# Kernel tuning notes

Hardware: AMD Instinct MI355X
Metric: run time of the kernel (lower is better)

Reference implementation:

```python
import jax, jax.numpy as jnp
import numpy as np

NL, D, Di, N, R, K, V, NH = 24, 768, 1536, 16, 48, 4, 50280, 12
BATCH, SEQ = 4, 256


def setup_inputs():
    key = jax.random.key(0)
    it = iter(jax.random.split(key, 48))
    g = lambda shape, s=0.02: jax.random.normal(next(it), shape, jnp.float32) * s
    inp = {
        "question_ids": jax.random.randint(next(it), (BATCH, SEQ), 0, V),
        "question_mask": jnp.ones((BATCH, SEQ), jnp.int32),
        "answer_ids": jax.random.randint(next(it), (BATCH, SEQ), 0, V),
        "answer_mask": jnp.ones((BATCH, SEQ), jnp.int32),
        "embed": g((V, D)),
        "norm_w": jnp.ones((NL, D)),
        "in_proj_w": g((NL, 2 * Di, D)),
        "conv_w": g((NL, Di, K), 0.1),
        "conv_b": jnp.zeros((NL, Di)),
        "x_proj_w": g((NL, R + 2 * N, Di)),
        "dt_proj_w": g((NL, Di, R)),
        "dt_proj_b": g((NL, Di), 0.5) - 4.0,
        "A_log": jnp.log(jnp.broadcast_to(jnp.arange(1, N + 1, dtype=jnp.float32), (NL, Di, N))) + 0.0,
        "D_p": jnp.ones((NL, Di)),
        "out_proj_w": g((NL, D, Di)),
        "norm_f": jnp.ones((D,)),
        "ln1_w": jnp.ones((D,)), "ln1_b": jnp.zeros((D,)),
        "qkv_w": g((3 * D, D)), "qkv_b": jnp.zeros((3 * D,)),
        "attn_out_w": g((D, D)), "attn_out_b": jnp.zeros((D,)),
        "ln2_w": jnp.ones((D,)), "ln2_b": jnp.zeros((D,)),
        "ff1_w": g((4 * D, D)), "ff1_b": jnp.zeros((4 * D,)),
        "ff2_w": g((D, 4 * D)), "ff2_b": jnp.zeros((D,)),
        "C_w": g((1, N)), "proj_out_w": g((D, Di)),
        "B_w": g((N, 1)), "proj_in_w": g((Di, D), 0.002),
    }
    return inp


def _rms(x, w, eps=1e-5):
    return x * jax.lax.rsqrt(jnp.mean(x * x, axis=-1, keepdims=True) + eps) * w


def _ln(x, w, b, eps=1e-5):
    m = jnp.mean(x, axis=-1, keepdims=True)
    v = jnp.var(x, axis=-1, keepdims=True)
    return (x - m) * jax.lax.rsqrt(v + eps) * w + b


def _mamba_block(h, layer, init_state):
    nw, ipw, cw, cb, xpw, dpw, dpb, alog, dp, opw = layer
    x_in = _rms(h, nw)
    xz = jnp.einsum('bld,ed->ble', x_in, ipw)  # (B,L,2*Di)
    x, z = jnp.split(xz, 2, axis=-1)
    L = x.shape[1]
    xp = jnp.pad(x, ((0, 0), (K - 1, 0), (0, 0)))  # causal depthwise conv, kernel K
    x = sum(xp[:, k:k + L, :] * cw[:, k] for k in range(K)) + cb
    x = jax.nn.silu(x)
    dbl = jnp.einsum('bld,ed->ble', x, xpw)
    dt, Bm, Cm = dbl[..., :R], dbl[..., R:R + N], dbl[..., R + N:]
    delta = jax.nn.softplus(jnp.einsum('blr,dr->bld', dt, dpw) + dpb)  # (B,L,Di)
    A = -jnp.exp(alog)  # (Di,N)

    def step(hs, t):  # selective scan, carry (B,Di,N)
        d_t, x_t, B_t, C_t = t
        hs = jnp.exp(d_t[..., None] * A) * hs + (d_t * x_t)[..., None] * B_t[:, None, :]
        return hs, jnp.einsum('bdn,bn->bd', hs, C_t)

    xs = tuple(jnp.moveaxis(a, 1, 0) for a in (delta, x, Bm, Cm))
    last, ys = jax.lax.scan(step, init_state, xs)
    y = jnp.moveaxis(ys, 0, 1) + x * dp
    y = y * jax.nn.silu(z)
    return h + jnp.einsum('bld,od->blo', y, opw), last


def _backbone(ids, mask, embed, mamba_params, norm_f, init_states):
    h = embed[ids] * mask[..., None].astype(embed.dtype)
    block = jax.checkpoint(_mamba_block)  # remat per layer: bounds bwd memory

    def layer_step(carry, xs):
        *layer, st = xs
        return block(carry, tuple(layer), st)

    h, lasts = jax.lax.scan(layer_step, h, mamba_params + (init_states,))
    h = _rms(h, norm_f)
    return jnp.einsum('bld,vd->blv', h, embed), lasts  # tied lm head


def _tf_layer(x, ln1_w, ln1_b, qkv_w, qkv_b, attn_out_w, attn_out_b, ln2_w, ln2_b, ff1_w, ff1_b, ff2_w, ff2_b):
    B, S, _ = x.shape
    hd = D // NH
    y = _ln(x, ln1_w, ln1_b)  # norm_first pre-LN
    q, k, v = jnp.split(y @ qkv_w.T + qkv_b, 3, axis=-1)
    q = q.reshape(B, S, NH, hd); k = k.reshape(B, S, NH, hd); v = v.reshape(B, S, NH, hd)
    att = jax.nn.softmax(jnp.einsum('bqhd,bkhd->bhqk', q, k) / jnp.sqrt(jnp.float32(hd)), axis=-1)
    o = jnp.einsum('bhqk,bkhd->bqhd', att, v).reshape(B, S, D)
    x = x + o @ attn_out_w.T + attn_out_b
    y = _ln(x, ln2_w, ln2_b)
    return x + jax.nn.gelu(y @ ff1_w.T + ff1_b, approximate=False) @ ff2_w.T + ff2_b


def _refine(states, C_w, proj_out_w, B_w, proj_in_w, tf_params):
    # states: (B, NL, Di, N); 12-step recurrent state refinement
    for _ in range(12):
        d = jnp.einsum('bsdn,n->bsd', states, C_w[0])  # C: Linear(16,1), squeeze(-1)
        d = jnp.einsum('bsd,od->bso', d, proj_out_w)   # 1536 -> 768
        d = _tf_layer(d, *tf_params)
        d = jnp.einsum('bso,do->bsd', d, proj_in_w)    # 768 -> 1536
        states = states + d[..., None] * B_w[:, 0]     # B: Linear(1,16)
    return states


def reference(question_ids, question_mask, answer_ids, answer_mask, embed, norm_w, in_proj_w, conv_w, conv_b, x_proj_w, dt_proj_w, dt_proj_b, A_log, D_p, out_proj_w, norm_f, ln1_w, ln1_b, qkv_w, qkv_b, attn_out_w, attn_out_b, ln2_w, ln2_b, ff1_w, ff1_b, ff2_w, ff2_b, C_w, proj_out_w, B_w, proj_in_w):
    mamba_params = (norm_w, in_proj_w, conv_w, conv_b, x_proj_w, dt_proj_w, dt_proj_b, A_log, D_p, out_proj_w)
    tf_params = (ln1_w, ln1_b, qkv_w, qkv_b, attn_out_w, attn_out_b, ln2_w, ln2_b, ff1_w, ff1_b, ff2_w, ff2_b)
    Bsz = question_ids.shape[0]
    zeros = jnp.zeros((NL, Bsz, Di, N), embed.dtype)
    _, lasts = _backbone(question_ids, question_mask, embed, mamba_params, norm_f, zeros)
    states = jnp.moveaxis(lasts, 0, 1)  # torch.stack(states, dim=1): (B, NL, Di, N)
    states = _refine(states, C_w, proj_out_w, B_w, proj_in_w, tf_params)
    logits, _ = _backbone(answer_ids, answer_mask, embed, mamba_params, norm_f, jnp.moveaxis(states, 0, 1))
    return logits
```

## Files before the change

### kernel.cpp

```cpp
#include <hip/hip_runtime.h>
#include <math.h>

namespace {

constexpr int kNL = 24, kD = 768, kDi = 1536, kN = 16, kR = 48, kK = 4, kV = 50280, kNH = 12;
constexpr int kB = 4, kS = 256;
constexpr int kMtok = kB * kS;
constexpr int kMref = kB * kNL;
constexpr int kVp = 50304;

using bf16x8 = __attribute__((ext_vector_type(8))) short;
using f32x4  = __attribute__((ext_vector_type(4))) float;

__device__ __forceinline__ float siluf(float x) { return x / (1.f + __expf(-x)); }

__device__ __forceinline__ ushort f2b(float f) {
    union { float f; unsigned u; } v; v.f = f;
    unsigned u = v.u;
    unsigned r = (u + 0x7FFFu + ((u >> 16) & 1u)) >> 16;
    return (ushort)r;
}

#define GLOAD_LDS(g, l) \
    __builtin_amdgcn_global_load_lds((const __attribute__((address_space(1))) void*)(g), \
                                     (__attribute__((address_space(3))) void*)(l), 16, 0, 0)

template <int BM, int BN, int BIAS, int ACT, int RES, int OUTMODE>
__global__ __launch_bounds__(256, ((BM + BN) <= 128 ? 4 : 2)) void gemm_bf16(
    const ushort* __restrict__ A, int lda,
    const ushort* __restrict__ B, int ldb,
    float* __restrict__ C, int ldc,
    ushort* __restrict__ Cbf, int ldcb,
    float* __restrict__ C2,
    const float* __restrict__ bias,
    int M, int N, int K)
{
    constexpr int ACH = BM / 32;
    constexpr int BCH = BN / 32;
    constexpr int MI  = BM / 32;
    constexpr int NJ  = BN / 32;

    __shared__ ushort As[2][BM * 64];
    __shared__ ushort Bs[2][BN * 64];

    const int tid  = threadIdx.x;
    const int lane = tid & 63;
    const int wave = tid >> 6;
    const int m0 = blockIdx.y * BM;
    const int n0 = blockIdx.x * BN;
    const int wr = (wave >> 1) * (BM / 2);
    const int wc = (wave & 1) * (BN / 2);

    f32x4 acc[MI][NJ];
#pragma unroll
    for (int i = 0; i < MI; ++i)
#pragma unroll
        for (int j = 0; j < NJ; ++j) acc[i][j] = f32x4{0.f, 0.f, 0.f, 0.f};

    const int srow = lane >> 3;
    const int scol = ((lane & 7) ^ srow) * 8;
    const ushort* gA[ACH];
    const ushort* gB[BCH];
#pragma unroll
    for (int g = 0; g < ACH; ++g)
        gA[g] = A + (size_t)(m0 + (g * 4 + wave) * 8 + srow) * lda + scol;
#pragma unroll
    for (int g = 0; g < BCH; ++g)
        gB[g] = B + (size_t)(n0 + (g * 4 + wave) * 8 + srow) * ldb + scol;

    const int frow = lane & 15;
    const int kh   = lane >> 4;
    const int nt   = K >> 6;

#pragma unroll
    for (int g = 0; g < ACH; ++g) GLOAD_LDS(gA[g], &As[0][(g * 4 + wave) * 512]);
#pragma unroll
    for (int g = 0; g < BCH; ++g) GLOAD_LDS(gB[g], &Bs[0][(g * 4 + wave) * 512]);
    __syncthreads();

    int cur = 0;
    for (int t = 0; t < nt; ++t) {
        if (t + 1 < nt) {
            const int off = (t + 1) * 64;
#pragma unroll
            for (int g = 0; g < ACH; ++g) GLOAD_LDS(gA[g] + off, &As[cur ^ 1][(g * 4 + wave) * 512]);
#pragma unroll
            for (int g = 0; g < BCH; ++g) GLOAD_LDS(gB[g] + off, &Bs[cur ^ 1][(g * 4 + wave) * 512]);
        }
#pragma unroll
        for (int s = 0; s < 2; ++s) {
            bf16x8 fa[MI], fb[NJ];
#pragma unroll
            for (int i = 0; i < MI; ++i) {
                int r = wr + i * 16 + frow;
                int slot = (s * 4 + kh) ^ (r & 7);
                fa[i] = *(const bf16x8*)&As[cur][r * 64 + slot * 8];
            }
#pragma unroll
            for (int j = 0; j < NJ; ++j) {
                int r = wc + j * 16 + frow;
                int slot = (s * 4 + kh) ^ (r & 7);
                fb[j] = *(const bf16x8*)&Bs[cur][r * 64 + slot * 8];
            }
#pragma unroll
            for (int i = 0; i < MI; ++i)
#pragma unroll
                for (int j = 0; j < NJ; ++j)
                    acc[i][j] = __builtin_amdgcn_mfma_f32_16x16x32_bf16(fa[i], fb[j], acc[i][j], 0, 0, 0);
        }
        __syncthreads();
        cur ^= 1;
    }

    const int ccol = lane & 15;
    const int crow = (lane >> 4) * 4;
#pragma unroll
    for (int i = 0; i < MI; ++i) {
#pragma unroll
        for (int j = 0; j < NJ; ++j) {
            int gn = n0 + wc + j * 16 + ccol;
            if (gn >= N) continue;
            float bv = BIAS ? bias[gn] : 0.f;
#pragma unroll
            for (int q = 0; q < 4; ++q) {
                int gm = m0 + wr + i * 16 + crow + q;
                if (gm >= M) continue;
                float v = acc[i][j][q] + bv;
                if (ACT == 1) v = fmaxf(v, 0.f) + log1pf(expf(-fabsf(v)));
                if (ACT == 2) v = 0.5f * v * (1.f + erff(v * 0.70710678118654752f));
                if (OUTMODE == 3) {
                    if (gn < 48) Cbf[(size_t)gm * 64 + gn] = f2b(v);
                    else if (gn < 64) { Cbf[(size_t)gm * 64 + gn] = 0; C2[(size_t)(gn - 48) * kMtok + gm] = v; }
                    else if (gn < 80) C2[(size_t)(gn - 48) * kMtok + gm] = v;
                } else if (OUTMODE == 4) {
                    C2[(size_t)gn * kMtok + gm] = v;
                } else if (OUTMODE == 5) {
                    if (gn < kDi) C[(size_t)gm * kDi + gn] = v;
                    else C2[(size_t)(gn - kDi) * kMtok + gm] = siluf(v);
                } else {
                    size_t ci = (size_t)gm * ldc + gn;
                    if (RES) v += C[ci];
                    if (OUTMODE != 2) C[ci] = v;
                    if (OUTMODE == 1 || OUTMODE == 2) Cbf[(size_t)gm * ldcb + gn] = f2b(v);
                }
            }
        }
    }
}

template <int BM, int BN, int BIAS, int ACT, int RES, int OUTMODE>
static void gemm(const ushort* A, int lda, const ushort* B, int ldb,
                 float* C, int ldc, ushort* Cb, int ldcb, float* C2,
                 const float* bias, int M, int N, int K, hipStream_t s)
{
    dim3 g((N + BN - 1) / BN, (M + BM - 1) / BM);
    gemm_bf16<BM, BN, BIAS, ACT, RES, OUTMODE><<<g, dim3(256), 0, s>>>(
        A, lda, B, ldb, C, ldc, Cb, ldcb, C2, bias, M, N, K);
}

__global__ void cvt_kernel(const float* __restrict__ src, ushort* __restrict__ dst, int n) {
    int i = (blockIdx.x * 256 + threadIdx.x) * 4;
    if (i >= n) return;
    float4 v = *(const float4*)(src + i);
    ushort4 o; o.x = f2b(v.x); o.y = f2b(v.y); o.z = f2b(v.z); o.w = f2b(v.w);
    *(ushort4*)(dst + i) = o;
}

__global__ void cvt_xpw_kernel(const float* __restrict__ src, ushort* __restrict__ dst) {
    int i = (blockIdx.x * 256 + threadIdx.x) * 4;
    if (i >= 24 * 80 * 1536) return;
    int l = i / (80 * 1536), r = i - l * (80 * 1536);
    int row = r / 1536, col = r - row * 1536;
    float4 v = *(const float4*)(src + i);
    ushort4 o; o.x = f2b(v.x); o.y = f2b(v.y); o.z = f2b(v.z); o.w = f2b(v.w);
    *(ushort4*)(dst + ((size_t)(l * 128 + row)) * 1536 + col) = o;
}

__global__ void cvt_dpw_kernel(const float* __restrict__ src, ushort* __restrict__ dst) {
    int i = blockIdx.x * 256 + threadIdx.x;
    if (i >= 24 * 1536 * 64) return;
    int col = i & 63, row = i >> 6;
    dst[i] = (col < 48) ? f2b(src[(size_t)row * 48 + col]) : (ushort)0;
}

__global__ void embed_kernel(const int* __restrict__ ids, const int* __restrict__ msk,
                             const float* __restrict__ embed, float* __restrict__ h)
{
    int i = blockIdx.x * 256 + threadIdx.x;
    int row = i / kD, col = i - row * kD;
    h[i] = embed[(size_t)ids[row] * kD + col] * (float)msk[row];
}

__global__ __launch_bounds__(256) void rms_kernel(const float* __restrict__ x,
                                                  const float* __restrict__ w,
                                                  ushort* __restrict__ out)
{
    __shared__ float red[256];
    int row = blockIdx.x, tid = threadIdx.x;
    const float* xr = x + (size_t)row * kD;
    float s = 0.f;
    for (int j = tid; j < kD; j += 256) { float v = xr[j]; s += v * v; }
    red[tid] = s; __syncthreads();
    for (int o = 128; o > 0; o >>= 1) { if (tid < o) red[tid] += red[tid + o]; __syncthreads(); }
    float rs = rsqrtf(red[0] / (float)kD + 1e-5f);
    for (int j = tid; j < kD; j += 256) out[(size_t)row * kD + j] = f2b(xr[j] * rs * w[j]);
}

__global__ __launch_bounds__(256) void ln_kernel(const float* __restrict__ x,
                                                 const float* __restrict__ w,
                                                 const float* __restrict__ b,
                                                 ushort* __restrict__ out)
{
    __shared__ float r1[256], r2[256];
    int row = blockIdx.x, tid = threadIdx.x;
    const float* xr = x + (size_t)row * kD;
    float s = 0.f, s2 = 0.f;
    for (int j = tid; j < kD; j += 256) { float v = xr[j]; s += v; s2 += v * v; }
    r1[tid] = s; r2[tid] = s2; __syncthreads();
    for (int o = 128; o > 0; o >>= 1) {
        if (tid < o) { r1[tid] += r1[tid + o]; r2[tid] += r2[tid + o]; }
        __syncthreads();
    }
    float mean = r1[0] / (float)kD;
    float var = r2[0] / (float)kD - mean * mean;
    float rs = rsqrtf(var + 1e-5f);
    for (int j = tid; j < kD; j += 256)
        out[(size_t)row * kD + j] = f2b((xr[j] - mean) * rs * w[j] + b[j]);
}

__global__ __launch_bounds__(256) void conv_kernel(
    const float* __restrict__ xbuf , const float* __restrict__ cw,
    const float* __restrict__ cb, ushort* __restrict__ xc_bf ,
    float* __restrict__ xcT )
{
    int d   = blockIdx.x * 256 + threadIdx.x;
    int bt0 = blockIdx.y * 16;
    int t0  = bt0 & (kS - 1);
    float w0 = cw[d * 4], w1 = cw[d * 4 + 1], w2 = cw[d * 4 + 2], w3 = cw[d * 4 + 3];
    float bias = cb[d];
    float xv[19];
#pragma unroll
    for (int j = 0; j < 19; ++j) {
        int tt = t0 - 3 + j;
        xv[j] = (tt >= 0) ? xbuf[(size_t)(bt0 - 3 + j) * kDi + d] : 0.f;
    }
    float out[16];
#pragma unroll
    for (int e = 0; e < 16; ++e) {
        float s = bias + xv[e] * w0 + xv[e + 1] * w1 + xv[e + 2] * w2 + xv[e + 3] * w3;
        float v = siluf(s);
        out[e] = v;
        xc_bf[(size_t)(bt0 + e) * kDi + d] = f2b(v);
    }
    float4* dst = (float4*)(xcT + (size_t)d * kMtok + bt0);
#pragma unroll
    for (int i = 0; i < 4; ++i)
        dst[i] = make_float4(out[i * 4], out[i * 4 + 1], out[i * 4 + 2], out[i * 4 + 3]);
}

__global__ __launch_bounds__(256) void scan_kernel(
    const float* __restrict__ dltT, const float* __restrict__ xcT,
    const float* __restrict__ zT, const float* __restrict__ bcT,
    const float* __restrict__ alog, const float* __restrict__ dp,
    float* __restrict__ states, ushort* __restrict__ y)
{
    int gid = blockIdx.x * 256 + threadIdx.x;
    int n = gid & 15;
    int d = (gid >> 4) % kDi;
    int b = gid / (kDi * kN);
    float Areg = -__expf(alog[d * kN + n]);
    float dpv = dp[d];
    size_t sidx = (size_t)(b * kDi + d) * kN + n;
    float hs = states[sidx];
    const float4* pD = (const float4*)(dltT + (size_t)d * kMtok + b * kS);
    const float4* pX = (const float4*)(xcT  + (size_t)d * kMtok + b * kS);
    const float4* pZ = (const float4*)(zT   + (size_t)d * kMtok + b * kS);
    const float4* pB = (const float4*)(bcT + (size_t)n * kMtok + b * kS);
    const float4* pC = (const float4*)(bcT + (size_t)(16 + n) * kMtok + b * kS);
    float4 D = pD[0], X = pX[0], Z = pZ[0], Bq = pB[0], Cq = pC[0];
    ushort* yrow = y + (size_t)(b * kS) * kDi + d;
    for (int g = 0; g < kS / 4; ++g) {
        float4 Dn, Xn, Zn, Bn, Cn;
        if (g + 1 < kS / 4) { Dn = pD[g + 1]; Xn = pX[g + 1]; Zn = pZ[g + 1]; Bn = pB[g + 1]; Cn = pC[g + 1]; }
#pragma unroll
        for (int e = 0; e < 4; ++e) {
            float dv = (&D.x)[e], xv = (&X.x)[e], zv = (&Z.x)[e];
            float Bv = (&Bq.x)[e], Cv = (&Cq.x)[e];
            hs = __expf(dv * Areg) * hs + (dv * xv) * Bv;
            float p = hs * Cv;
            p += __shfl_xor(p, 1, 16);
            p += __shfl_xor(p, 2, 16);
            p += __shfl_xor(p, 4, 16);
            p += __shfl_xor(p, 8, 16);
            if (n == 0) yrow[(size_t)(g * 4 + e) * kDi] = f2b((p + xv * dpv) * zv);
        }
        D = Dn; X = Xn; Z = Zn; Bq = Bn; Cq = Cn;
    }
    states[sidx] = hs;
}

__global__ void contract_kernel(const float* __restrict__ st, const float* __restrict__ Cw,
                                ushort* __restrict__ dDi)
{
    int i = blockIdx.x * 256 + threadIdx.x;
    int row = i / kDi, di = i - row * kDi;
    int b = row / kNL, s = row - b * kNL;
    const float* sp = st + ((size_t)(s * kB + b) * kDi + di) * kN;
    float acc = 0.f;
#pragma unroll
    for (int nn = 0; nn < kN; ++nn) acc += sp[nn] * Cw[nn];
    dDi[i] = f2b(acc);
}

__global__ void update_contract_kernel(const float* __restrict__ d1536,
                                       const float* __restrict__ Bw,
                                       float* __restrict__ st,
                                       const float* __restrict__ Cw,
                                       ushort* __restrict__ dDi)
{
    int i = blockIdx.x * 256 + threadIdx.x;
    int row = i / kDi, di = i - row * kDi;
    int b = row / kNL, s = row - b * kNL;
    float dv = d1536[i];
    float* sp = st + ((size_t)(s * kB + b) * kDi + di) * kN;
    float acc = 0.f;
#pragma unroll
    for (int nn = 0; nn < kN; ++nn) {
        float v = sp[nn] + dv * Bw[nn];
        sp[nn] = v;
        acc += v * Cw[nn];
    }
    dDi[i] = f2b(acc);
}

__global__ __launch_bounds__(32) void attn_kernel(const float* __restrict__ qkv,
                                                  ushort* __restrict__ o)
{
    int b = blockIdx.x / kNH;
    int hh = blockIdx.x - b * kNH;
    int sq = threadIdx.x;
    if (sq >= kNL) return;
    const float* qrow = qkv + (size_t)(b * kNL + sq) * (3 * kD) + hh * 64;
    float q[64];
#pragma unroll
    for (int e = 0; e < 64; ++e) q[e] = qrow[e];
    float sc[kNL];
    float mx = -1e30f;
    for (int sk = 0; sk < kNL; ++sk) {
        const float* krow = qkv + (size_t)(b * kNL + sk) * (3 * kD) + kD + hh * 64;
        float dt = 0.f;
#pragma unroll
        for (int e = 0; e < 64; ++e) dt += q[e] * krow[e];
        dt *= 0.125f;
        sc[sk] = dt;
        mx = fmaxf(mx, dt);
    }
    float sum = 0.f;
    for (int sk = 0; sk < kNL; ++sk) { sc[sk] = expf(sc[sk] - mx); sum += sc[sk]; }
    float inv = 1.f / sum;
    float out[64];
#pragma unroll
    for (int e = 0; e < 64; ++e) out[e] = 0.f;
    for (int sk = 0; sk < kNL; ++sk) {
        float wgt = sc[sk] * inv;
        const float* vrow = qkv + (size_t)(b * kNL + sk) * (3 * kD) + 2 * kD + hh * 64;
#pragma unroll
        for (int e = 0; e < 64; ++e) out[e] += wgt * vrow[e];
    }
    ushort* orow = o + (size_t)(b * kNL + sq) * kD + hh * 64;
#pragma unroll
    for (int e = 0; e < 64; ++e) orow[e] = f2b(out[e]);
}

}

extern "C" void kernel_launch(void* const* d_in, const int* in_sizes, int n_in,
                              void* d_out, int out_size, void* d_ws, size_t ws_size,
                              hipStream_t stream)
{
    const int*   q_ids  = (const int*)d_in[0];
    const int*   q_msk  = (const int*)d_in[1];
    const int*   a_ids  = (const int*)d_in[2];
    const int*   a_msk  = (const int*)d_in[3];
    const float* embed  = (const float*)d_in[4];
    const float* norm_w = (const float*)d_in[5];
    const float* ipw    = (const float*)d_in[6];
    const float* cw     = (const float*)d_in[7];
    const float* cb     = (const float*)d_in[8];
    const float* xpw    = (const float*)d_in[9];
    const float* dpw    = (const float*)d_in[10];
    const float* dpb    = (const float*)d_in[11];
    const float* alog   = (const float*)d_in[12];
    const float* dpp    = (const float*)d_in[13];
    const float* opw    = (const float*)d_in[14];
    const float* norm_f = (const float*)d_in[15];
    const float* ln1w   = (const float*)d_in[16];
    const float* ln1b   = (const float*)d_in[17];
    const float* qkvw   = (const float*)d_in[18];
    const float* qkvbi  = (const float*)d_in[19];
    const float* aow    = (const float*)d_in[20];
    const float* aob    = (const float*)d_in[21];
    const float* ln2w   = (const float*)d_in[22];
    const float* ln2b   = (const float*)d_in[23];
    const float* ff1w   = (const float*)d_in[24];
    const float* ff1b   = (const float*)d_in[25];
    const float* ff2w   = (const float*)d_in[26];
    const float* ff2b   = (const float*)d_in[27];
    const float* Cwp    = (const float*)d_in[28];
    const float* powp   = (const float*)d_in[29];
    const float* Bwp    = (const float*)d_in[30];
    const float* piwp   = (const float*)d_in[31];

    char* base = (char*)d_ws;
    size_t cur = 0;
    auto allocB = [&](size_t bytes) { char* p = base + cur; cur = (cur + bytes + 255) & ~(size_t)255; return p; };
    auto allocF = [&](size_t n) { return (float*)allocB(n * 4); };
    auto allocH = [&](size_t n) { return (ushort*)allocB(n * 2); };

    float* h     = allocF((size_t)kMtok * kD);
    float* xbuf  = allocF((size_t)kMtok * kDi);
    float* zT    = allocF((size_t)kDi * kMtok);
    float* xcT   = allocF((size_t)kDi * kMtok);
    float* bcT   = allocF((size_t)32 * kMtok);
    float* dltT  = allocF((size_t)kDi * kMtok);
    float* st    = allocF((size_t)kNL * kB * kDi * kN);
    float* x768  = allocF((size_t)kMref * kD);
    float* qkvB  = allocF((size_t)kMref * 3 * kD);
    float* d1536 = allocF((size_t)kMref * kDi);
    ushort* xin_bf  = allocH((size_t)kMtok * kD);
    ushort* xc_bf   = allocH((size_t)kMtok * kDi);
    ushort* dtin_bf = allocH((size_t)kMtok * 64);
    ushort* yb_bf   = allocH((size_t)kMtok * kDi);
    ushort* dDi_bf  = allocH((size_t)128 * kDi);
    ushort* tb_bf   = allocH((size_t)128 * kD);
    ushort* o768_bf = allocH((size_t)128 * kD);
    ushort* f3_bf   = allocH((size_t)128 * 4 * kD);
    ushort* x768_bf = allocH((size_t)128 * kD);
    ushort* xpw_bf  = allocH((size_t)kNL * 128 * kDi);
    ushort* dpw_bf  = allocH((size_t)kNL * kDi * 64);
    ushort* powp_bf = allocH((size_t)kD * kDi);
    ushort* qkvw_bf = allocH((size_t)3 * kD * kD);
    ushort* aow_bf  = allocH((size_t)kD * kD);
    ushort* ff1w_bf = allocH((size_t)4 * kD * kD);
    ushort* ff2w_bf = allocH((size_t)kD * 4 * kD);
    ushort* piw_bf  = allocH((size_t)kDi * kD);
    ushort* emb_bf  = allocH((size_t)kVp * kD);

    size_t base_end = cur;
    ushort* ipw_all = allocH((size_t)kNL * 2 * kDi * kD);
    ushort* opw_all = allocH((size_t)kNL * kD * kDi);
    bool full = (cur <= ws_size);
    ushort* ipw_stg = nullptr;
    ushort* opw_stg = nullptr;
    if (!full) {
        cur = base_end;
        ipw_stg = allocH((size_t)2 * kDi * kD);
        opw_stg = allocH((size_t)kD * kDi);
        if (cur > ws_size) return;
    }

    auto cvt = [&](const float* s, ushort* d, size_t n) {
        cvt_kernel<<<dim3((unsigned)((n / 4 + 255) / 256)), dim3(256), 0, stream>>>(s, d, (int)n);
    };

    hipMemsetAsync(st, 0, sizeof(float) * (size_t)kNL * kB * kDi * kN, stream);

    cvt_xpw_kernel<<<dim3(2880), dim3(256), 0, stream>>>(xpw, xpw_bf);
    cvt_dpw_kernel<<<dim3(9216), dim3(256), 0, stream>>>(dpw, dpw_bf);
    cvt(powp, powp_bf, (size_t)kD * kDi);
    cvt(qkvw, qkvw_bf, (size_t)3 * kD * kD);
    cvt(aow,  aow_bf,  (size_t)kD * kD);
    cvt(ff1w, ff1w_bf, (size_t)4 * kD * kD);
    cvt(ff2w, ff2w_bf, (size_t)kD * 4 * kD);
    cvt(piwp, piw_bf,  (size_t)kDi * kD);
    cvt(embed, emb_bf, (size_t)kV * kD);
    if (full) {
        cvt(ipw, ipw_all, (size_t)kNL * 2 * kDi * kD);
        cvt(opw, opw_all, (size_t)kNL * kD * kDi);
    }

    for (int pass = 0; pass < 2; ++pass) {
        const int* ids = pass ? a_ids : q_ids;
        const int* msk = pass ? a_msk : q_msk;

        embed_kernel<<<dim3(kMtok * kD / 256), dim3(256), 0, stream>>>(ids, msk, embed, h);

        for (int l = 0; l < kNL; ++l) {
            const ushort* ipw_l;
            const ushort* opw_l;
            if (full) {
                ipw_l = ipw_all + (size_t)l * 2 * kDi * kD;
                opw_l = opw_all + (size_t)l * kD * kDi;
            } else {
                cvt(ipw + (size_t)l * 2 * kDi * kD, ipw_stg, (size_t)2 * kDi * kD);
                cvt(opw + (size_t)l * kD * kDi, opw_stg, (size_t)kD * kDi);
                ipw_l = ipw_stg;
                opw_l = opw_stg;
            }
            rms_kernel<<<dim3(kMtok), dim3(256), 0, stream>>>(h, norm_w + (size_t)l * kD, xin_bf);
            gemm<128, 128, 0, 0, 0, 5>(xin_bf, kD, ipw_l, kD, xbuf, kDi, nullptr, 0, zT,
                                       nullptr, kMtok, 2 * kDi, kD, stream);
            conv_kernel<<<dim3(kDi / 256, kMtok / 16), dim3(256), 0, stream>>>(
                xbuf, cw + (size_t)l * kDi * kK, cb + (size_t)l * kDi, xc_bf, xcT);
            gemm<64, 64, 0, 0, 0, 3>(xc_bf, kDi, xpw_bf + (size_t)l * 128 * kDi, kDi,
                                     nullptr, 0, dtin_bf, 0, bcT, nullptr, kMtok, 128, kDi, stream);
            gemm<64, 64, 1, 1, 0, 4>(dtin_bf, 64, dpw_bf + (size_t)l * kDi * 64, 64,
                                     nullptr, 0, nullptr, 0, dltT,
                                     dpb + (size_t)l * kDi, kMtok, kDi, 64, stream);
            scan_kernel<<<dim3(kB * kDi * kN / 256), dim3(256), 0, stream>>>(
                dltT, xcT, zT, bcT, alog + (size_t)l * kDi * kN, dpp + (size_t)l * kDi,
                st + (size_t)l * kB * kDi * kN, yb_bf);
            gemm<64, 64, 0, 0, 1, 0>(yb_bf, kDi, opw_l, kDi, h, kD, nullptr, 0, nullptr,
                                     nullptr, kMtok, kD, kDi, stream);
        }

        if (pass == 0) {
            contract_kernel<<<dim3(kMref * kDi / 256), dim3(256), 0, stream>>>(st, Cwp, dDi_bf);
            for (int it = 0; it < 12; ++it) {
                gemm<64, 64, 0, 0, 0, 0>(dDi_bf, kDi, powp_bf, kDi, x768, kD, nullptr, 0, nullptr,
                                         nullptr, kMref, kD, kDi, stream);
                ln_kernel<<<dim3(kMref), dim3(256), 0, stream>>>(x768, ln1w, ln1b, tb_bf);
                gemm<64, 64, 1, 0, 0, 0>(tb_bf, kD, qkvw_bf, kD, qkvB, 3 * kD, nullptr, 0, nullptr,
                                         qkvbi, kMref, 3 * kD, kD, stream);
                attn_kernel<<<dim3(kB * kNH), dim3(32), 0, stream>>>(qkvB, o768_bf);
                gemm<64, 64, 1, 0, 1, 0>(o768_bf, kD, aow_bf, kD, x768, kD, nullptr, 0, nullptr,
                                         aob, kMref, kD, kD, stream);
                ln_kernel<<<dim3(kMref), dim3(256), 0, stream>>>(x768, ln2w, ln2b, tb_bf);
                gemm<64, 64, 1, 2, 0, 2>(tb_bf, kD, ff1w_bf, kD, nullptr, 0, f3_bf, 4 * kD, nullptr,
                                         ff1b, kMref, 4 * kD, kD, stream);
                gemm<64, 64, 1, 0, 1, 1>(f3_bf, 4 * kD, ff2w_bf, 4 * kD, x768, kD, x768_bf, kD, nullptr,
                                         ff2b, kMref, kD, 4 * kD, stream);
                gemm<64, 64, 0, 0, 0, 0>(x768_bf, kD, piw_bf, kD, d1536, kDi, nullptr, 0, nullptr,
                                         nullptr, kMref, kDi, kD, stream);
                update_contract_kernel<<<dim3(kMref * kDi / 256), dim3(256), 0, stream>>>(
                    d1536, Bwp, st, Cwp, dDi_bf);
            }
        } else {
            rms_kernel<<<dim3(kMtok), dim3(256), 0, stream>>>(h, norm_f, xin_bf);
            gemm<128, 128, 0, 0, 0, 0>(xin_bf, kD, emb_bf, kD, (float*)d_out, kV, nullptr, 0, nullptr,
                                       nullptr, kMtok, kV, kD, stream);
        }
    }
}
```

Baseline: 9.360 ms.

## Fold dt_proj into x_proj weights, fuse state update, add triple-buffered GEMM

```diff
diff --git a/kernel.cpp b/kernel.cpp
--- a/kernel.cpp
+++ b/kernel.cpp
@@ -8,6 +8,8 @@
 constexpr int kMtok = kB * kS;
 constexpr int kMref = kB * kNL;
 constexpr int kVp = 50304;
+constexpr int kNx = 1568;
+constexpr int kNxPad = 1600;
 
 using bf16x8 = __attribute__((ext_vector_type(8))) short;
 using f32x4  = __attribute__((ext_vector_type(4))) float;
@@ -25,14 +27,15 @@
     __builtin_amdgcn_global_load_lds((const __attribute__((address_space(1))) void*)(g), \
                                      (__attribute__((address_space(3))) void*)(l), 16, 0, 0)
 
-template <int BM, int BN, int BIAS, int ACT, int RES, int OUTMODE>
-__global__ __launch_bounds__(256, ((BM + BN) <= 128 ? 4 : 2)) void gemm_bf16(
+template <int BM, int BN, int BIAS, int ACT, int RES, int OUTMODE, int PIPE>
+__global__ __launch_bounds__(256, (PIPE == 3 ? 3 : 2)) void gemm_bf16(
     const ushort* __restrict__ A, int lda,
     const ushort* __restrict__ B, int ldb,
     float* __restrict__ C, int ldc,
     ushort* __restrict__ Cbf, int ldcb,
     float* __restrict__ C2,
     const float* __restrict__ bias,
+    const float* __restrict__ aux,
     int M, int N, int K)
 {
     constexpr int ACH = BM / 32;
@@ -40,8 +43,8 @@
     constexpr int MI  = BM / 32;
     constexpr int NJ  = BN / 32;
 
-    __shared__ ushort As[2][BM * 64];
-    __shared__ ushort Bs[2][BN * 64];
+    __shared__ ushort As[PIPE][BM * 64];
+    __shared__ ushort Bs[PIPE][BN * 64];
 
     const int tid  = threadIdx.x;
     const int lane = tid & 63;
@@ -72,21 +75,14 @@
     const int kh   = lane >> 4;
     const int nt   = K >> 6;
 
-#pragma unroll
-    for (int g = 0; g < ACH; ++g) GLOAD_LDS(gA[g], &As[0][(g * 4 + wave) * 512]);
-#pragma unroll
-    for (int g = 0; g < BCH; ++g) GLOAD_LDS(gB[g], &Bs[0][(g * 4 + wave) * 512]);
-    __syncthreads();
-
-    int cur = 0;
-    for (int t = 0; t < nt; ++t) {
-        if (t + 1 < nt) {
-            const int off = (t + 1) * 64;
-#pragma unroll
-            for (int g = 0; g < ACH; ++g) GLOAD_LDS(gA[g] + off, &As[cur ^ 1][(g * 4 + wave) * 512]);
-#pragma unroll
-            for (int g = 0; g < BCH; ++g) GLOAD_LDS(gB[g] + off, &Bs[cur ^ 1][(g * 4 + wave) * 512]);
-        }
+    auto stage = [&](int t, int buf) {
+        const int off = t * 64;
+#pragma unroll
+        for (int g = 0; g < ACH; ++g) GLOAD_LDS(gA[g] + off, &As[buf][(g * 4 + wave) * 512]);
+#pragma unroll
+        for (int g = 0; g < BCH; ++g) GLOAD_LDS(gB[g] + off, &Bs[buf][(g * 4 + wave) * 512]);
+    };
+    auto compute = [&](int buf) {
 #pragma unroll
         for (int s = 0; s < 2; ++s) {
             bf16x8 fa[MI], fb[NJ];
@@ -94,13 +90,13 @@
             for (int i = 0; i < MI; ++i) {
                 int r = wr + i * 16 + frow;
                 int slot = (s * 4 + kh) ^ (r & 7);
-                fa[i] = *(const bf16x8*)&As[cur][r * 64 + slot * 8];
+                fa[i] = *(const bf16x8*)&As[buf][r * 64 + slot * 8];
             }
 #pragma unroll
             for (int j = 0; j < NJ; ++j) {
                 int r = wc + j * 16 + frow;
                 int slot = (s * 4 + kh) ^ (r & 7);
-                fb[j] = *(const bf16x8*)&Bs[cur][r * 64 + slot * 8];
+                fb[j] = *(const bf16x8*)&Bs[buf][r * 64 + slot * 8];
             }
 #pragma unroll
             for (int i = 0; i < MI; ++i)
@@ -108,8 +104,32 @@
                 for (int j = 0; j < NJ; ++j)
                     acc[i][j] = __builtin_amdgcn_mfma_f32_16x16x32_bf16(fa[i], fb[j], acc[i][j], 0, 0, 0);
         }
+    };
+
+    if constexpr (PIPE == 3) {
+        stage(0, 0);
+        if (nt > 1) stage(1, 1);
+        for (int t = 0; t < nt; ++t) {
+            if (t < nt - 1) {
+                asm volatile("s_waitcnt vmcnt(%0)" :: "n"(ACH + BCH) : "memory");
+            } else {
+                asm volatile("s_waitcnt vmcnt(0)" ::: "memory");
+            }
+            __builtin_amdgcn_s_barrier();
+            if (t + 2 < nt) stage(t + 2, (t + 2) % 3);
+            compute(t % 3);
+        }
+        __builtin_amdgcn_s_barrier();
+    } else {
+        stage(0, 0);
         __syncthreads();
-        cur ^= 1;
+        int cur = 0;
+        for (int t = 0; t < nt; ++t) {
+            if (t + 1 < nt) stage(t + 1, cur ^ 1);
+            compute(cur);
+            __syncthreads();
+            cur ^= 1;
+        }
     }
 
     const int ccol = lane & 15;
@@ -128,15 +148,27 @@
                 float v = acc[i][j][q] + bv;
                 if (ACT == 1) v = fmaxf(v, 0.f) + log1pf(expf(-fabsf(v)));
                 if (ACT == 2) v = 0.5f * v * (1.f + erff(v * 0.70710678118654752f));
-                if (OUTMODE == 3) {
-                    if (gn < 48) Cbf[(size_t)gm * 64 + gn] = f2b(v);
-                    else if (gn < 64) { Cbf[(size_t)gm * 64 + gn] = 0; C2[(size_t)(gn - 48) * kMtok + gm] = v; }
-                    else if (gn < 80) C2[(size_t)(gn - 48) * kMtok + gm] = v;
-                } else if (OUTMODE == 4) {
-                    C2[(size_t)gn * kMtok + gm] = v;
-                } else if (OUTMODE == 5) {
+                if (OUTMODE == 5) {
                     if (gn < kDi) C[(size_t)gm * kDi + gn] = v;
                     else C2[(size_t)(gn - kDi) * kMtok + gm] = siluf(v);
+                } else if (OUTMODE == 6) {
+                    if (gn < 32) C2[(size_t)gn * kMtok + gm] = v;
+                    else {
+                        float w = v + bias[gn - 32];
+                        w = fmaxf(w, 0.f) + log1pf(expf(-fabsf(w)));
+                        C[(size_t)(gn - 32) * kMtok + gm] = w;
+                    }
+                } else if (OUTMODE == 7) {
+                    int bb = gm / kNL, ss = gm - bb * kNL;
+                    float* stp = C2 + ((size_t)(ss * kB + bb) * kDi + gn) * kN;
+                    float a2 = 0.f;
+#pragma unroll
+                    for (int nn = 0; nn < kN; ++nn) {
+                        float sv = stp[nn] + v * bias[nn];
+                        stp[nn] = sv;
+                        a2 += sv * aux[nn];
+                    }
+                    Cbf[(size_t)gm * ldcb + gn] = f2b(a2);
                 } else {
                     size_t ci = (size_t)gm * ldc + gn;
                     if (RES) v += C[ci];
@@ -148,14 +180,14 @@
     }
 }
 
-template <int BM, int BN, int BIAS, int ACT, int RES, int OUTMODE>
+template <int BM, int BN, int BIAS, int ACT, int RES, int OUTMODE, int PIPE>
 static void gemm(const ushort* A, int lda, const ushort* B, int ldb,
                  float* C, int ldc, ushort* Cb, int ldcb, float* C2,
-                 const float* bias, int M, int N, int K, hipStream_t s)
+                 const float* bias, const float* aux, int M, int N, int K, hipStream_t s)
 {
     dim3 g((N + BN - 1) / BN, (M + BM - 1) / BM);
-    gemm_bf16<BM, BN, BIAS, ACT, RES, OUTMODE><<<g, dim3(256), 0, s>>>(
-        A, lda, B, ldb, C, ldc, Cb, ldcb, C2, bias, M, N, K);
+    gemm_bf16<BM, BN, BIAS, ACT, RES, OUTMODE, PIPE><<<g, dim3(256), 0, s>>>(
+        A, lda, B, ldb, C, ldc, Cb, ldcb, C2, bias, aux, M, N, K);
 }
 
 __global__ void cvt_kernel(const float* __restrict__ src, ushort* __restrict__ dst, int n) {
@@ -166,21 +198,29 @@
     *(ushort4*)(dst + i) = o;
 }
 
-__global__ void cvt_xpw_kernel(const float* __restrict__ src, ushort* __restrict__ dst) {
-    int i = (blockIdx.x * 256 + threadIdx.x) * 4;
-    if (i >= 24 * 80 * 1536) return;
-    int l = i / (80 * 1536), r = i - l * (80 * 1536);
-    int row = r / 1536, col = r - row * 1536;
-    float4 v = *(const float4*)(src + i);
-    ushort4 o; o.x = f2b(v.x); o.y = f2b(v.y); o.z = f2b(v.z); o.w = f2b(v.w);
-    *(ushort4*)(dst + ((size_t)(l * 128 + row)) * 1536 + col) = o;
-}
-
 __global__ void cvt_dpw_kernel(const float* __restrict__ src, ushort* __restrict__ dst) {
     int i = blockIdx.x * 256 + threadIdx.x;
     if (i >= 24 * 1536 * 64) return;
     int col = i & 63, row = i >> 6;
     dst[i] = (col < 48) ? f2b(src[(size_t)row * 48 + col]) : (ushort)0;
+}
+
+__global__ void cvt_xpwdtT_kernel(const float* __restrict__ src, ushort* __restrict__ dst) {
+    int i = blockIdx.x * 256 + threadIdx.x;
+    if (i >= 24 * 1536 * 64) return;
+    int r = i & 63;
+    int j = (i >> 6) % 1536;
+    int l = i / (1536 * 64);
+    dst[i] = (r < 48) ? f2b(src[((size_t)l * 80 + r) * 1536 + j]) : (ushort)0;
+}
+
+__global__ void cvt_bc_kernel(const float* __restrict__ src, ushort* __restrict__ dst) {
+    int i = blockIdx.x * 256 + threadIdx.x;
+    if (i >= 24 * 32 * 1536) return;
+    int k = i % 1536;
+    int gn = (i / 1536) % 32;
+    int l = i / (32 * 1536);
+    dst[((size_t)l * kNxPad + gn) * 1536 + k] = f2b(src[((size_t)l * 80 + 48 + gn) * 1536 + k]);
 }
 
 __global__ void embed_kernel(const int* __restrict__ ids, const int* __restrict__ msk,
@@ -229,9 +269,9 @@
 }
 
 __global__ __launch_bounds__(256) void conv_kernel(
-    const float* __restrict__ xbuf , const float* __restrict__ cw,
-    const float* __restrict__ cb, ushort* __restrict__ xc_bf ,
-    float* __restrict__ xcT )
+    const float* __restrict__ xbuf, const float* __restrict__ cw,
+    const float* __restrict__ cb, ushort* __restrict__ xc_bf,
+    float* __restrict__ xcT)
 {
     int d   = blockIdx.x * 256 + threadIdx.x;
     int bt0 = blockIdx.y * 16;
@@ -309,27 +349,6 @@
     float acc = 0.f;
 #pragma unroll
     for (int nn = 0; nn < kN; ++nn) acc += sp[nn] * Cw[nn];
-    dDi[i] = f2b(acc);
-}
-
-__global__ void update_contract_kernel(const float* __restrict__ d1536,
-                                       const float* __restrict__ Bw,
-                                       float* __restrict__ st,
-                                       const float* __restrict__ Cw,
-                                       ushort* __restrict__ dDi)
-{
-    int i = blockIdx.x * 256 + threadIdx.x;
-    int row = i / kDi, di = i - row * kDi;
-    int b = row / kNL, s = row - b * kNL;
-    float dv = d1536[i];
-    float* sp = st + ((size_t)(s * kB + b) * kDi + di) * kN;
-    float acc = 0.f;
-#pragma unroll
-    for (int nn = 0; nn < kN; ++nn) {
-        float v = sp[nn] + dv * Bw[nn];
-        sp[nn] = v;
-        acc += v * Cw[nn];
-    }
     dDi[i] = f2b(acc);
 }
 
@@ -426,18 +445,17 @@
     float* st    = allocF((size_t)kNL * kB * kDi * kN);
     float* x768  = allocF((size_t)kMref * kD);
     float* qkvB  = allocF((size_t)kMref * 3 * kD);
-    float* d1536 = allocF((size_t)kMref * kDi);
     ushort* xin_bf  = allocH((size_t)kMtok * kD);
     ushort* xc_bf   = allocH((size_t)kMtok * kDi);
-    ushort* dtin_bf = allocH((size_t)kMtok * 64);
     ushort* yb_bf   = allocH((size_t)kMtok * kDi);
     ushort* dDi_bf  = allocH((size_t)128 * kDi);
     ushort* tb_bf   = allocH((size_t)128 * kD);
     ushort* o768_bf = allocH((size_t)128 * kD);
     ushort* f3_bf   = allocH((size_t)128 * 4 * kD);
     ushort* x768_bf = allocH((size_t)128 * kD);
-    ushort* xpw_bf  = allocH((size_t)kNL * 128 * kDi);
+    ushort* xpw2    = allocH((size_t)kNL * kNxPad * kDi);
     ushort* dpw_bf  = allocH((size_t)kNL * kDi * 64);
+    ushort* xpwdtT  = allocH((size_t)kNL * kDi * 64);
     ushort* powp_bf = allocH((size_t)kD * kDi);
     ushort* qkvw_bf = allocH((size_t)3 * kD * kD);
     ushort* aow_bf  = allocH((size_t)kD * kD);
@@ -464,9 +482,18 @@
     };
 
     hipMemsetAsync(st, 0, sizeof(float) * (size_t)kNL * kB * kDi * kN, stream);
-
-    cvt_xpw_kernel<<<dim3(2880), dim3(256), 0, stream>>>(xpw, xpw_bf);
+    hipMemsetAsync(xpw2, 0, sizeof(ushort) * (size_t)kNL * kNxPad * kDi, stream);
+
     cvt_dpw_kernel<<<dim3(9216), dim3(256), 0, stream>>>(dpw, dpw_bf);
+    cvt_xpwdtT_kernel<<<dim3(9216), dim3(256), 0, stream>>>(xpw, xpwdtT);
+    cvt_bc_kernel<<<dim3(4608), dim3(256), 0, stream>>>(xpw, xpw2);
+    for (int l = 0; l < kNL; ++l) {
+        gemm<64, 64, 0, 0, 0, 2, 3>(dpw_bf + (size_t)l * kDi * 64, 64,
+                                    xpwdtT + (size_t)l * kDi * 64, 64,
+                                    nullptr, 0,
+                                    xpw2 + (size_t)l * kNxPad * kDi + 32 * kDi, kDi,
+                                    nullptr, nullptr, nullptr, kDi, kDi, 64, stream);
+    }
     cvt(powp, powp_bf, (size_t)kD * kDi);
     cvt(qkvw, qkvw_bf, (size_t)3 * kD * kD);
     cvt(aow,  aow_bf,  (size_t)kD * kD);
@@ -498,47 +525,43 @@
                 opw_l = opw_stg;
             }
             rms_kernel<<<dim3(kMtok), dim3(256), 0, stream>>>(h, norm_w + (size_t)l * kD, xin_bf);
-            gemm<128, 128, 0, 0, 0, 5>(xin_bf, kD, ipw_l, kD, xbuf, kDi, nullptr, 0, zT,
-                                       nullptr, kMtok, 2 * kDi, kD, stream);
+            gemm<64, 64, 0, 0, 0, 5, 3>(xin_bf, kD, ipw_l, kD, xbuf, kDi, nullptr, 0, zT,
+                                        nullptr, nullptr, kMtok, 2 * kDi, kD, stream);
             conv_kernel<<<dim3(kDi / 256, kMtok / 16), dim3(256), 0, stream>>>(
                 xbuf, cw + (size_t)l * kDi * kK, cb + (size_t)l * kDi, xc_bf, xcT);
-            gemm<64, 64, 0, 0, 0, 3>(xc_bf, kDi, xpw_bf + (size_t)l * 128 * kDi, kDi,
-                                     nullptr, 0, dtin_bf, 0, bcT, nullptr, kMtok, 128, kDi, stream);
-            gemm<64, 64, 1, 1, 0, 4>(dtin_bf, 64, dpw_bf + (size_t)l * kDi * 64, 64,
-                                     nullptr, 0, nullptr, 0, dltT,
-                                     dpb + (size_t)l * kDi, kMtok, kDi, 64, stream);
+            gemm<64, 64, 0, 0, 0, 6, 3>(xc_bf, kDi, xpw2 + (size_t)l * kNxPad * kDi, kDi,
+                                        dltT, 0, nullptr, 0, bcT,
+                                        dpb + (size_t)l * kDi, nullptr, kMtok, kNx, kDi, stream);
             scan_kernel<<<dim3(kB * kDi * kN / 256), dim3(256), 0, stream>>>(
                 dltT, xcT, zT, bcT, alog + (size_t)l * kDi * kN, dpp + (size_t)l * kDi,
                 st + (size_t)l * kB * kDi * kN, yb_bf);
-            gemm<64, 64, 0, 0, 1, 0>(yb_bf, kDi, opw_l, kDi, h, kD, nullptr, 0, nullptr,
-                                     nullptr, kMtok, kD, kDi, stream);
+            gemm<64, 64, 0, 0, 1, 0, 3>(yb_bf, kDi, opw_l, kDi, h, kD, nullptr, 0, nullptr,
+                                        nullptr, nullptr, kMtok, kD, kDi, stream);
         }
 
         if (pass == 0) {
             contract_kernel<<<dim3(kMref * kDi / 256), dim3(256), 0, stream>>>(st, Cwp, dDi_bf);
             for (int it = 0; it < 12; ++it) {
-                gemm<64, 64, 0, 0, 0, 0>(dDi_bf, kDi, powp_bf, kDi, x768, kD, nullptr, 0, nullptr,
-                                         nullptr, kMref, kD, kDi, stream);
+                gemm<64, 64, 0, 0, 0, 0, 3>(dDi_bf, kDi, powp_bf, kDi, x768, kD, nullptr, 0, nullptr,
+                                            nullptr, nullptr, kMref, kD, kDi, stream);
                 ln_kernel<<<dim3(kMref), dim3(256), 0, stream>>>(x768, ln1w, ln1b, tb_bf);
-                gemm<64, 64, 1, 0, 0, 0>(tb_bf, kD, qkvw_bf, kD, qkvB, 3 * kD, nullptr, 0, nullptr,
-                                         qkvbi, kMref, 3 * kD, kD, stream);
+                gemm<64, 64, 1, 0, 0, 0, 3>(tb_bf, kD, qkvw_bf, kD, qkvB, 3 * kD, nullptr, 0, nullptr,
+                                            qkvbi, nullptr, kMref, 3 * kD, kD, stream);
                 attn_kernel<<<dim3(kB * kNH), dim3(32), 0, stream>>>(qkvB, o768_bf);
-                gemm<64, 64, 1, 0, 1, 0>(o768_bf, kD, aow_bf, kD, x768, kD, nullptr, 0, nullptr,
-                                         aob, kMref, kD, kD, stream);
+                gemm<64, 64, 1, 0, 1, 0, 3>(o768_bf, kD, aow_bf, kD, x768, kD, nullptr, 0, nullptr,
+                                            aob, nullptr, kMref, kD, kD, stream);
                 ln_kernel<<<dim3(kMref), dim3(256), 0, stream>>>(x768, ln2w, ln2b, tb_bf);
-                gemm<64, 64, 1, 2, 0, 2>(tb_bf, kD, ff1w_bf, kD, nullptr, 0, f3_bf, 4 * kD, nullptr,
-                                         ff1b, kMref, 4 * kD, kD, stream);
-                gemm<64, 64, 1, 0, 1, 1>(f3_bf, 4 * kD, ff2w_bf, 4 * kD, x768, kD, x768_bf, kD, nullptr,
-                                         ff2b, kMref, kD, 4 * kD, stream);
-                gemm<64, 64, 0, 0, 0, 0>(x768_bf, kD, piw_bf, kD, d1536, kDi, nullptr, 0, nullptr,
-                                         nullptr, kMref, kDi, kD, stream);
-                update_contract_kernel<<<dim3(kMref * kDi / 256), dim3(256), 0, stream>>>(
-                    d1536, Bwp, st, Cwp, dDi_bf);
+                gemm<64, 64, 1, 2, 0, 2, 3>(tb_bf, kD, ff1w_bf, kD, nullptr, 0, f3_bf, 4 * kD, nullptr,
+                                            ff1b, nullptr, kMref, 4 * kD, kD, stream);
+                gemm<64, 64, 1, 0, 1, 1, 3>(f3_bf, 4 * kD, ff2w_bf, 4 * kD, x768, kD, x768_bf, kD, nullptr,
+                                            ff2b, nullptr, kMref, kD, 4 * kD, stream);
+                gemm<64, 64, 0, 0, 0, 7, 3>(x768_bf, kD, piw_bf, kD, nullptr, 0, dDi_bf, kDi, st,
+                                            Bwp, Cwp, kMref, kDi, kD, stream);
             }
         } else {
             rms_kernel<<<dim3(kMtok), dim3(256), 0, stream>>>(h, norm_f, xin_bf);
-            gemm<128, 128, 0, 0, 0, 0>(xin_bf, kD, emb_bf, kD, (float*)d_out, kV, nullptr, 0, nullptr,
-                                       nullptr, kMtok, kV, kD, stream);
-        }
-    }
-}
+            gemm<128, 128, 0, 0, 0, 0, 2>(xin_bf, kD, emb_bf, kD, (float*)d_out, kV, nullptr, 0, nullptr,
+                                          nullptr, nullptr, kMtok, kV, kD, stream);
+        }
+    }
+}
```

New measurement: 9.255 ms. About the same (-1.1%).
